# Optimization experiments

Hardware: AMD Instinct MI355X
Metric: run time of the kernel (lower is better)

## Reference

```python
import jax, jax.numpy as jnp
import numpy as np

B, S, D, H, W = 2, 2048, 1024, 16, 128
HD = D // H
EPS = 1e-5
NEG = -1e9


def setup_inputs() -> dict:
    key = jax.random.key(0)
    ks = jax.random.split(key, 6)
    sd = 1.0 / np.sqrt(D)
    return {
        "x": jax.random.normal(ks[0], (B, S, D), jnp.float32),
        "Wq": jax.random.normal(ks[1], (D, D), jnp.float32) * sd,
        "bq": jnp.zeros((D,), jnp.float32),
        "Wk": jax.random.normal(ks[2], (D, D), jnp.float32) * sd,
        "bk": jnp.zeros((D,), jnp.float32),
        "Wv": jax.random.normal(ks[3], (D, D), jnp.float32) * sd,
        "bv": jnp.zeros((D,), jnp.float32),
        "Wo": jax.random.normal(ks[4], (D, D), jnp.float32) * sd,
        "bo": jnp.zeros((D,), jnp.float32),
        "gamma": jnp.ones((D,), jnp.float32),
        "beta": jnp.zeros((D,), jnp.float32),
    }


def _local_causal_mask(seq_len, window):
    pos = jnp.arange(seq_len)
    qp = pos[:, None]
    kp = pos[None, :]
    return (jnp.abs(qp - kp) < window) & (qp >= kp)  # [S, S] bool


def reference(x, Wq, bq, Wk, bk, Wv, bv, Wo, bo, gamma, beta):
    scale = 1.0 / np.sqrt(HD)
    # projections -> [B, H, S, HD]
    def split_heads(t):
        return t.reshape(B, S, H, HD).transpose(0, 2, 1, 3)

    q = split_heads(x @ Wq + bq)
    k = split_heads(x @ Wk + bk)
    v = split_heads(x @ Wv + bv)

    scores = jnp.einsum("bhqd,bhkd->bhqk", q, k) * scale  # [B,H,S,S]
    mask = _local_causal_mask(S, W)
    scores = jnp.where(mask[None, None, :, :], scores, NEG)
    attn = jax.nn.softmax(scores, axis=-1)
    out = jnp.einsum("bhqk,bhkd->bhqd", attn, v)  # [B,H,S,HD]
    out = out.transpose(0, 2, 1, 3).reshape(B, S, D)
    out = out @ Wo + bo

    # residual + LayerNorm(eps=1e-5)
    y = x + out
    mu = jnp.mean(y, axis=-1, keepdims=True)
    var = jnp.mean(jnp.square(y - mu), axis=-1, keepdims=True)
    y = (y - mu) * jax.lax.rsqrt(var + EPS) * gamma + beta
    return y
```

## Files before the change

kernel.cpp:

```cpp
#include <hip/hip_runtime.h>
#include <hip/hip_bf16.h>

typedef __hip_bfloat16 bf16;
typedef float f32x4 __attribute__((ext_vector_type(4)));
typedef short bf16x8 __attribute__((ext_vector_type(8)));
typedef int   int4v  __attribute__((ext_vector_type(4)));

constexpr int Bb = 2, Ss = 2048, Dd = 1024, Hh = 16, Ww = 128, HDd = 64;
constexpr int Mrows = Bb * Ss;

__device__ __forceinline__ void gload16(const void* g, void* l) {
  __builtin_amdgcn_global_load_lds(
      (const __attribute__((address_space(1))) void*)g,
      (__attribute__((address_space(3))) void*)l, 16, 0, 0);
}

__device__ __forceinline__ f32x4 mfma16(bf16x8 a, bf16x8 b, f32x4 c) {
  return __builtin_amdgcn_mfma_f32_16x16x32_bf16(a, b, c, 0, 0, 0);
}

__global__ __launch_bounds__(256) void convert_bf16_k(const float* __restrict__ in,
                                                      bf16* __restrict__ out) {
  size_t i = (size_t)blockIdx.x * 256 + threadIdx.x;
  float4 v = reinterpret_cast<const float4*>(in)[i];
  union { bf16 b[4]; ushort4 u; } cv;
  cv.b[0] = __float2bfloat16(v.x);
  cv.b[1] = __float2bfloat16(v.y);
  cv.b[2] = __float2bfloat16(v.z);
  cv.b[3] = __float2bfloat16(v.w);
  reinterpret_cast<ushort4*>(out)[i] = cv.u;
}

__global__ __launch_bounds__(256) void transpose_w4_k(const float* __restrict__ W0,
                                                      const float* __restrict__ W1,
                                                      const float* __restrict__ W2,
                                                      const float* __restrict__ W3,
                                                      bf16* __restrict__ out) {
  const float* Win = (blockIdx.z == 0) ? W0 : (blockIdx.z == 1) ? W1
                     : (blockIdx.z == 2) ? W2 : W3;
  bf16* o = out + (size_t)blockIdx.z * Dd * Dd;
  __shared__ float tile[32][33];
  int bx = blockIdx.x, by = blockIdx.y;
  int tx = threadIdx.x & 31, ty = threadIdx.x >> 5;
#pragma unroll
  for (int i = 0; i < 4; ++i)
    tile[ty + i * 8][tx] = Win[(size_t)(by * 32 + ty + i * 8) * Dd + bx * 32 + tx];
  __syncthreads();
#pragma unroll
  for (int i = 0; i < 4; ++i)
    o[(size_t)(bx * 32 + ty + i * 8) * Dd + by * 32 + tx] =
        __float2bfloat16(tile[tx][ty + i * 8]);
}

__device__ __forceinline__ void gemm_core8(const bf16* __restrict__ A,
                                           const bf16* __restrict__ Bt,
                                           int bm, int bn,
                                           bf16* As, bf16* Bs, f32x4 acc[2][4]) {
  const int t = threadIdx.x;
  const int lane = t & 63, w = t >> 6;
  const int wr = w >> 1, wc = w & 1;
  const int l15 = lane & 15, l16 = lane >> 4;
  const bf16* Arow0 = A + (size_t)bm * 128 * Dd;
  const bf16* Brow0 = Bt + (size_t)bn * 128 * Dd;

  for (int kt = 0; kt < Dd / 64; ++kt) {
    __syncthreads();
#pragma unroll
    for (int i = 0; i < 2; ++i) {
      int ci = i * 512 + t;
      int row = ci >> 3, pc = ci & 7;
      int sc = pc ^ (row & 7);
      gload16(Arow0 + (size_t)row * Dd + kt * 64 + sc * 8, As + ci * 8);
      gload16(Brow0 + (size_t)row * Dd + kt * 64 + sc * 8, Bs + ci * 8);
    }
    __syncthreads();
    bf16x8 af[2][2], bfr[4][2];
#pragma unroll
    for (int m = 0; m < 2; ++m) {
      int row = wr * 32 + m * 16 + l15;
#pragma unroll
      for (int kk = 0; kk < 2; ++kk)
        af[m][kk] = *reinterpret_cast<const bf16x8*>(
            As + row * 64 + (((kk * 4 + l16) ^ (row & 7)) * 8));
    }
#pragma unroll
    for (int n = 0; n < 4; ++n) {
      int row = wc * 64 + n * 16 + l15;
#pragma unroll
      for (int kk = 0; kk < 2; ++kk)
        bfr[n][kk] = *reinterpret_cast<const bf16x8*>(
            Bs + row * 64 + (((kk * 4 + l16) ^ (row & 7)) * 8));
    }
    __builtin_amdgcn_s_setprio(1);
#pragma unroll
    for (int m = 0; m < 2; ++m)
#pragma unroll
      for (int n = 0; n < 4; ++n) {
        acc[m][n] = mfma16(af[m][0], bfr[n][0], acc[m][n]);
        acc[m][n] = mfma16(af[m][1], bfr[n][1], acc[m][n]);
      }
    __builtin_amdgcn_s_setprio(0);
  }
}

__global__ __launch_bounds__(512) void gemm_qkv8w(const bf16* __restrict__ A,
                                                  const bf16* __restrict__ Wt3,
                                                  const float* __restrict__ bq,
                                                  const float* __restrict__ bk,
                                                  const float* __restrict__ bv,
                                                  bf16* __restrict__ Qh,
                                                  bf16* __restrict__ Kh,
                                                  bf16* __restrict__ Vt) {
  __shared__ bf16 As[128 * 64], Bs[128 * 64];
  __shared__ bf16 rep[8][16][72];
  f32x4 acc[2][4] = {};
  int id = blockIdx.x;
  int wg = (id & 7) * 96 + (id >> 3);
  int bm = wg / 24, bn = wg % 24;
  gemm_core8(A, Wt3, bm, bn, As, Bs, acc);

  const int lane = threadIdx.x & 63, w = threadIdx.x >> 6;
  const int wr = w >> 1, wc = w & 1, l15 = lane & 15, l16 = lane >> 4;
  const int p = bn >> 3;
  const int c0w = (bn & 7) * 128 + wc * 64;
  const int h = c0w >> 6;

  if (p < 2) {
    bf16* dst = p ? Kh : Qh;
    const float* bp = p ? bk : bq;
    float bi[4];
#pragma unroll
    for (int n = 0; n < 4; ++n) bi[n] = bp[c0w + n * 16 + l15];
#pragma unroll
    for (int m = 0; m < 2; ++m) {
#pragma unroll
      for (int n = 0; n < 4; ++n)
#pragma unroll
        for (int r = 0; r < 4; ++r)
          rep[w][l16 * 4 + r][n * 16 + l15] = __float2bfloat16(acc[m][n][r] + bi[n]);
      int rrow = lane >> 2, rch = lane & 3;
      int sg = bm * 128 + wr * 32 + m * 16 + rrow;
      int b = sg >> 11, sl = sg & (Ss - 1);
      bf16* base = dst + (((size_t)(b * Hh + h)) * Ss + sl) * HDd;
      bf16x8 v0 = *reinterpret_cast<const bf16x8*>(&rep[w][rrow][rch * 8]);
      bf16x8 v1 = *reinterpret_cast<const bf16x8*>(&rep[w][rrow][(rch + 4) * 8]);
      *reinterpret_cast<bf16x8*>(base + rch * 8) = v0;
      *reinterpret_cast<bf16x8*>(base + (rch + 4) * 8) = v1;
    }
  } else {
#pragma unroll
    for (int n = 0; n < 4; ++n) {
      int col = c0w + n * 16 + l15;
      int hh = col >> 6, hd = col & (HDd - 1);
      float bi = bv[col];
#pragma unroll
      for (int m = 0; m < 2; ++m) {
        int s0 = bm * 128 + wr * 32 + m * 16 + l16 * 4;
        int b = s0 >> 11, sl = s0 & (Ss - 1);
        union { ushort4 u; ushort e[4]; } pk;
#pragma unroll
        for (int r = 0; r < 4; ++r) {
          bf16 tb = __float2bfloat16(acc[m][n][r] + bi);
          pk.e[r] = *reinterpret_cast<ushort*>(&tb);
        }
        *reinterpret_cast<ushort4*>(&Vt[(((size_t)(b * Hh + hh)) * HDd + hd) * Ss + sl]) = pk.u;
      }
    }
  }
}

__global__ __launch_bounds__(512) void gemm_o8w(const bf16* __restrict__ AO,
                                                const bf16* __restrict__ WtO,
                                                const float* __restrict__ bo,
                                                const float* __restrict__ resid,
                                                float* __restrict__ out) {
  __shared__ bf16 As[128 * 64], Bs[128 * 64];
  f32x4 acc[2][4] = {};
  int id = blockIdx.x;
  int wg = (id & 7) * 32 + (id >> 3);
  int bm = wg >> 3, bn = wg & 7;
  gemm_core8(AO, WtO, bm, bn, As, Bs, acc);

  const int lane = threadIdx.x & 63, w = threadIdx.x >> 6;
  const int wr = w >> 1, wc = w & 1, l15 = lane & 15, l16 = lane >> 4;
#pragma unroll
  for (int m = 0; m < 2; ++m)
#pragma unroll
    for (int n = 0; n < 4; ++n) {
      int col = bn * 128 + wc * 64 + n * 16 + l15;
      float bi = bo[col];
#pragma unroll
      for (int r = 0; r < 4; ++r) {
        int row = bm * 128 + wr * 32 + m * 16 + l16 * 4 + r;
        size_t idx = (size_t)row * Dd + col;
        out[idx] = acc[m][n][r] + bi + resid[idx];
      }
    }
}

__global__ __launch_bounds__(256) void attn_local(const bf16* __restrict__ Q,
                                                  const bf16* __restrict__ K,
                                                  const bf16* __restrict__ Vt,
                                                  bf16* __restrict__ AO) {
  __shared__ bf16 Ps[4][16][200];
  const int t = threadIdx.x, lane = t & 63, w = t >> 6;
  const int l15 = lane & 15, l16 = lane >> 4;
  const int qb = blockIdx.x, h = blockIdx.y, b = blockIdx.z;
  const int q0 = qb * 64, kstart = q0 - 128;
  const bf16* Qp = Q + ((size_t)(b * Hh + h)) * Ss * HDd;
  const bf16* Kp = K + ((size_t)(b * Hh + h)) * Ss * HDd;
  const bf16* Vp = Vt + ((size_t)(b * Hh + h)) * HDd * Ss;

  const int qrow = q0 + w * 16 + l15;
  bf16x8 aq0 = *reinterpret_cast<const bf16x8*>(Qp + (size_t)qrow * HDd + l16 * 8);
  bf16x8 aq1 = *reinterpret_cast<const bf16x8*>(Qp + (size_t)qrow * HDd + 32 + l16 * 8);

  f32x4 sc[9];
  __builtin_amdgcn_s_setprio(1);
#pragma unroll
  for (int j = 0; j < 9; ++j) {
    int key = kstart + (w + j) * 16 + l15;
    int kc = key < 0 ? 0 : key;
    bf16x8 bk0 = *reinterpret_cast<const bf16x8*>(Kp + (size_t)kc * HDd + l16 * 8);
    bf16x8 bk1 = *reinterpret_cast<const bf16x8*>(Kp + (size_t)kc * HDd + 32 + l16 * 8);
    f32x4 s = {};
    s = mfma16(aq0, bk0, s);
    s = mfma16(aq1, bk1, s);
    sc[j] = s;
  }
  __builtin_amdgcn_s_setprio(0);

  const float scale = 0.125f;
  float mrow[4], ssum[4], inv[4];
  int qg[4];
#pragma unroll
  for (int r = 0; r < 4; ++r) { mrow[r] = -1e30f; qg[r] = q0 + w * 16 + l16 * 4 + r; }
#pragma unroll
  for (int j = 0; j < 9; ++j) {
    int kg = kstart + (w + j) * 16 + l15;
#pragma unroll
    for (int r = 0; r < 4; ++r) {
      bool valid = (kg >= 0) && (kg <= qg[r]) && (qg[r] - kg < Ww);
      float v = valid ? sc[j][r] * scale : -1e9f;
      sc[j][r] = v;
      mrow[r] = fmaxf(mrow[r], v);
    }
  }
#pragma unroll
  for (int r = 0; r < 4; ++r)
#pragma unroll
    for (int off = 1; off < 16; off <<= 1)
      mrow[r] = fmaxf(mrow[r], __shfl_xor(mrow[r], off));
#pragma unroll
  for (int r = 0; r < 4; ++r) ssum[r] = 0.f;
#pragma unroll
  for (int j = 0; j < 9; ++j)
#pragma unroll
    for (int r = 0; r < 4; ++r) {
      float p = __expf(sc[j][r] - mrow[r]);
      sc[j][r] = p;
      ssum[r] += p;
    }
#pragma unroll
  for (int r = 0; r < 4; ++r)
#pragma unroll
    for (int off = 1; off < 16; off <<= 1)
      ssum[r] += __shfl_xor(ssum[r], off);
#pragma unroll
  for (int r = 0; r < 4; ++r) inv[r] = 1.f / ssum[r];

#pragma unroll
  for (int j = 0; j < 9; ++j)
#pragma unroll
    for (int r = 0; r < 4; ++r)
      Ps[w][l16 * 4 + r][(w + j) * 16 + l15] = __float2bfloat16(sc[j][r]);
  {
    int ktz = (w & 1) ? (w - 1) : (w + 9);
    bf16 z16 = __float2bfloat16(0.f);
#pragma unroll
    for (int r = 0; r < 4; ++r)
      Ps[w][l16 * 4 + r][ktz * 16 + l15] = z16;
  }

  const int c0 = w >> 1;
  f32x4 o[4] = {};
  __builtin_amdgcn_s_setprio(1);
#pragma unroll
  for (int cc = 0; cc < 5; ++cc) {
    int c = c0 + cc;
    bf16x8 pf = *reinterpret_cast<const bf16x8*>(&Ps[w][l15][c * 32 + l16 * 8]);
    int kk = kstart + c * 32 + l16 * 8;
    int kc = kk < 0 ? 0 : kk;
#pragma unroll
    for (int ht = 0; ht < 4; ++ht) {
      bf16x8 vf = *reinterpret_cast<const bf16x8*>(Vp + (size_t)(ht * 16 + l15) * Ss + kc);
      o[ht] = mfma16(pf, vf, o[ht]);
    }
  }
  __builtin_amdgcn_s_setprio(0);

#pragma unroll
  for (int ht = 0; ht < 4; ++ht)
#pragma unroll
    for (int r = 0; r < 4; ++r) {
      int qw = q0 + w * 16 + l16 * 4 + r;
      int col = h * HDd + ht * 16 + l15;
      AO[(size_t)(b * Ss + qw) * Dd + col] = __float2bfloat16(o[ht][r] * inv[r]);
    }
}

__global__ __launch_bounds__(256) void ln_inplace(float* __restrict__ y,
                                                  const float* __restrict__ gamma,
                                                  const float* __restrict__ beta) {
  int row = blockIdx.x;
  float* yr = y + (size_t)row * Dd;
  float4 v = reinterpret_cast<const float4*>(yr)[threadIdx.x];
  float s = v.x + v.y + v.z + v.w;
  float s2 = v.x * v.x + v.y * v.y + v.z * v.z + v.w * v.w;
#pragma unroll
  for (int off = 1; off < 64; off <<= 1) {
    s += __shfl_xor(s, off);
    s2 += __shfl_xor(s2, off);
  }
  __shared__ float r1[4], r2[4];
  int w = threadIdx.x >> 6;
  if ((threadIdx.x & 63) == 0) { r1[w] = s; r2[w] = s2; }
  __syncthreads();
  s = r1[0] + r1[1] + r1[2] + r1[3];
  s2 = r2[0] + r2[1] + r2[2] + r2[3];
  float mu = s * (1.f / Dd);
  float var = s2 * (1.f / Dd) - mu * mu;
  float rs = rsqrtf(var + 1e-5f);
  float4 g = reinterpret_cast<const float4*>(gamma)[threadIdx.x];
  float4 be = reinterpret_cast<const float4*>(beta)[threadIdx.x];
  float4 o;
  o.x = (v.x - mu) * rs * g.x + be.x;
  o.y = (v.y - mu) * rs * g.y + be.y;
  o.z = (v.z - mu) * rs * g.z + be.z;
  o.w = (v.w - mu) * rs * g.w + be.w;
  reinterpret_cast<float4*>(yr)[threadIdx.x] = o;
}

extern "C" void kernel_launch(void* const* d_in, const int* in_sizes, int n_in,
                              void* d_out, int out_size, void* d_ws, size_t ws_size,
                              hipStream_t stream) {
  const float* x     = (const float*)d_in[0];
  const float* Wq    = (const float*)d_in[1];
  const float* bq    = (const float*)d_in[2];
  const float* Wk    = (const float*)d_in[3];
  const float* bk    = (const float*)d_in[4];
  const float* Wv    = (const float*)d_in[5];
  const float* bv    = (const float*)d_in[6];
  const float* Wo    = (const float*)d_in[7];
  const float* bo    = (const float*)d_in[8];
  const float* gamma = (const float*)d_in[9];
  const float* beta  = (const float*)d_in[10];
  float* out = (float*)d_out;

  char* ws = (char*)d_ws;
  bf16* xb  = (bf16*)(ws + (size_t)0);
  bf16* Wt3 = (bf16*)(ws + ((size_t)8  << 20));
  bf16* WtO = (bf16*)(ws + ((size_t)14 << 20));
  bf16* Qh  = (bf16*)(ws + ((size_t)16 << 20));
  bf16* Kh  = (bf16*)(ws + ((size_t)24 << 20));
  bf16* Vt  = (bf16*)(ws + ((size_t)32 << 20));
  bf16* AO  = (bf16*)(ws + ((size_t)40 << 20));

  convert_bf16_k<<<Mrows * Dd / (256 * 4), 256, 0, stream>>>(x, xb);
  transpose_w4_k<<<dim3(32, 32, 4), 256, 0, stream>>>(Wq, Wk, Wv, Wo, Wt3);

  gemm_qkv8w<<<768, 512, 0, stream>>>(xb, Wt3, bq, bk, bv, Qh, Kh, Vt);

  attn_local<<<dim3(Ss / 64, Hh, Bb), 256, 0, stream>>>(Qh, Kh, Vt, AO);

  gemm_o8w<<<256, 512, 0, stream>>>(AO, WtO, bo, x, out);
  ln_inplace<<<Mrows, 256, 0, stream>>>(out, gamma, beta);
}
```

Before: 103.3 us.

## Double-buffer GEMM LDS tiles and prefetch V fragments before softmax

The shared GEMM core now uses two LDS buffers, issuing the global-to-LDS loads for the next K tile while MFMAs run on the current one, with one barrier per iteration instead of two. The QKV epilogue's staging buffer is carved out of the same LDS block. The attention kernel issues the first three chunks of V loads into registers before the softmax, so that load latency overlaps the masking and reduction work. In exchange LDS per block doubles to 64KB, which may lower occupancy, and the V prefetch adds 48 VGPRs.

Measured after the change: 98.83 us. 4.3% less time.

```diff
diff --git a/kernel.cpp b/kernel.cpp
--- a/kernel.cpp
+++ b/kernel.cpp
@@ -8,6 +8,7 @@
 
 constexpr int Bb = 2, Ss = 2048, Dd = 1024, Hh = 16, Ww = 128, HDd = 64;
 constexpr int Mrows = Bb * Ss;
+constexpr int NTk = Dd / 64;
 
 __device__ __forceinline__ void gload16(const void* g, void* l) {
   __builtin_amdgcn_global_load_lds(
@@ -55,7 +56,7 @@
 __device__ __forceinline__ void gemm_core8(const bf16* __restrict__ A,
                                            const bf16* __restrict__ Bt,
                                            int bm, int bn,
-                                           bf16* As, bf16* Bs, f32x4 acc[2][4]) {
+                                           bf16* lds, f32x4 acc[2][4]) {
   const int t = threadIdx.x;
   const int lane = t & 63, w = t >> 6;
   const int wr = w >> 1, wc = w & 1;
@@ -63,25 +64,32 @@
   const bf16* Arow0 = A + (size_t)bm * 128 * Dd;
   const bf16* Brow0 = Bt + (size_t)bn * 128 * Dd;
 
-  for (int kt = 0; kt < Dd / 64; ++kt) {
-    __syncthreads();
+  auto stage = [&](int buf, int kt) {
 #pragma unroll
     for (int i = 0; i < 2; ++i) {
       int ci = i * 512 + t;
       int row = ci >> 3, pc = ci & 7;
       int sc = pc ^ (row & 7);
-      gload16(Arow0 + (size_t)row * Dd + kt * 64 + sc * 8, As + ci * 8);
-      gload16(Brow0 + (size_t)row * Dd + kt * 64 + sc * 8, Bs + ci * 8);
-    }
-    __syncthreads();
+      gload16(Arow0 + (size_t)row * Dd + kt * 64 + sc * 8, lds + buf * 16384 + ci * 8);
+      gload16(Brow0 + (size_t)row * Dd + kt * 64 + sc * 8, lds + buf * 16384 + 8192 + ci * 8);
+    }
+  };
+
+  stage(0, 0);
+  __syncthreads();
+  int buf = 0;
+  for (int kt = 0; kt < NTk; ++kt) {
+    if (kt + 1 < NTk) stage(buf ^ 1, kt + 1);
     bf16x8 af[2][2], bfr[4][2];
+    const bf16* Ab = lds + buf * 16384;
+    const bf16* Bb = Ab + 8192;
 #pragma unroll
     for (int m = 0; m < 2; ++m) {
       int row = wr * 32 + m * 16 + l15;
 #pragma unroll
       for (int kk = 0; kk < 2; ++kk)
         af[m][kk] = *reinterpret_cast<const bf16x8*>(
-            As + row * 64 + (((kk * 4 + l16) ^ (row & 7)) * 8));
+            Ab + row * 64 + (((kk * 4 + l16) ^ (row & 7)) * 8));
     }
 #pragma unroll
     for (int n = 0; n < 4; ++n) {
@@ -89,7 +97,7 @@
 #pragma unroll
       for (int kk = 0; kk < 2; ++kk)
         bfr[n][kk] = *reinterpret_cast<const bf16x8*>(
-            Bs + row * 64 + (((kk * 4 + l16) ^ (row & 7)) * 8));
+            Bb + row * 64 + (((kk * 4 + l16) ^ (row & 7)) * 8));
     }
     __builtin_amdgcn_s_setprio(1);
 #pragma unroll
@@ -100,6 +108,8 @@
         acc[m][n] = mfma16(af[m][1], bfr[n][1], acc[m][n]);
       }
     __builtin_amdgcn_s_setprio(0);
+    __syncthreads();
+    buf ^= 1;
   }
 }
 
@@ -111,13 +121,12 @@
                                                   bf16* __restrict__ Qh,
                                                   bf16* __restrict__ Kh,
                                                   bf16* __restrict__ Vt) {
-  __shared__ bf16 As[128 * 64], Bs[128 * 64];
-  __shared__ bf16 rep[8][16][72];
+  __shared__ __align__(16) bf16 lds[32768];
   f32x4 acc[2][4] = {};
   int id = blockIdx.x;
   int wg = (id & 7) * 96 + (id >> 3);
   int bm = wg / 24, bn = wg % 24;
-  gemm_core8(A, Wt3, bm, bn, As, Bs, acc);
+  gemm_core8(A, Wt3, bm, bn, lds, acc);
 
   const int lane = threadIdx.x & 63, w = threadIdx.x >> 6;
   const int wr = w >> 1, wc = w & 1, l15 = lane & 15, l16 = lane >> 4;
@@ -126,6 +135,7 @@
   const int h = c0w >> 6;
 
   if (p < 2) {
+    bf16 (*rep)[72] = reinterpret_cast<bf16(*)[72]>(lds + w * (16 * 72));
     bf16* dst = p ? Kh : Qh;
     const float* bp = p ? bk : bq;
     float bi[4];
@@ -137,13 +147,13 @@
       for (int n = 0; n < 4; ++n)
 #pragma unroll
         for (int r = 0; r < 4; ++r)
-          rep[w][l16 * 4 + r][n * 16 + l15] = __float2bfloat16(acc[m][n][r] + bi[n]);
+          rep[l16 * 4 + r][n * 16 + l15] = __float2bfloat16(acc[m][n][r] + bi[n]);
       int rrow = lane >> 2, rch = lane & 3;
       int sg = bm * 128 + wr * 32 + m * 16 + rrow;
       int b = sg >> 11, sl = sg & (Ss - 1);
       bf16* base = dst + (((size_t)(b * Hh + h)) * Ss + sl) * HDd;
-      bf16x8 v0 = *reinterpret_cast<const bf16x8*>(&rep[w][rrow][rch * 8]);
-      bf16x8 v1 = *reinterpret_cast<const bf16x8*>(&rep[w][rrow][(rch + 4) * 8]);
+      bf16x8 v0 = *reinterpret_cast<const bf16x8*>(&rep[rrow][rch * 8]);
+      bf16x8 v1 = *reinterpret_cast<const bf16x8*>(&rep[rrow][(rch + 4) * 8]);
       *reinterpret_cast<bf16x8*>(base + rch * 8) = v0;
       *reinterpret_cast<bf16x8*>(base + (rch + 4) * 8) = v1;
     }
@@ -174,12 +184,12 @@
                                                 const float* __restrict__ bo,
                                                 const float* __restrict__ resid,
                                                 float* __restrict__ out) {
-  __shared__ bf16 As[128 * 64], Bs[128 * 64];
+  __shared__ __align__(16) bf16 lds[32768];
   f32x4 acc[2][4] = {};
   int id = blockIdx.x;
   int wg = (id & 7) * 32 + (id >> 3);
   int bm = wg >> 3, bn = wg & 7;
-  gemm_core8(AO, WtO, bm, bn, As, Bs, acc);
+  gemm_core8(AO, WtO, bm, bn, lds, acc);
 
   const int lane = threadIdx.x & 63, w = threadIdx.x >> 6;
   const int wr = w >> 1, wc = w & 1, l15 = lane & 15, l16 = lane >> 4;
@@ -230,6 +240,17 @@
   }
   __builtin_amdgcn_s_setprio(0);
 
+  const int c0 = w >> 1;
+  bf16x8 vpre[3][4];
+#pragma unroll
+  for (int cc = 0; cc < 3; ++cc) {
+    int kk = kstart + (c0 + cc) * 32 + l16 * 8;
+    int kc = kk < 0 ? 0 : kk;
+#pragma unroll
+    for (int ht = 0; ht < 4; ++ht)
+      vpre[cc][ht] = *reinterpret_cast<const bf16x8*>(Vp + (size_t)(ht * 16 + l15) * Ss + kc);
+  }
+
   const float scale = 0.125f;
   float mrow[4], ssum[4], inv[4];
   int qg[4];
@@ -282,19 +303,24 @@
       Ps[w][l16 * 4 + r][ktz * 16 + l15] = z16;
   }
 
-  const int c0 = w >> 1;
   f32x4 o[4] = {};
   __builtin_amdgcn_s_setprio(1);
 #pragma unroll
   for (int cc = 0; cc < 5; ++cc) {
     int c = c0 + cc;
     bf16x8 pf = *reinterpret_cast<const bf16x8*>(&Ps[w][l15][c * 32 + l16 * 8]);
-    int kk = kstart + c * 32 + l16 * 8;
-    int kc = kk < 0 ? 0 : kk;
-#pragma unroll
-    for (int ht = 0; ht < 4; ++ht) {
-      bf16x8 vf = *reinterpret_cast<const bf16x8*>(Vp + (size_t)(ht * 16 + l15) * Ss + kc);
-      o[ht] = mfma16(pf, vf, o[ht]);
+    if (cc < 3) {
+#pragma unroll
+      for (int ht = 0; ht < 4; ++ht)
+        o[ht] = mfma16(pf, vpre[cc][ht], o[ht]);
+    } else {
+      int kk = kstart + c * 32 + l16 * 8;
+      int kc = kk < 0 ? 0 : kk;
+#pragma unroll
+      for (int ht = 0; ht < 4; ++ht) {
+        bf16x8 vf = *reinterpret_cast<const bf16x8*>(Vp + (size_t)(ht * 16 + l15) * Ss + kc);
+        o[ht] = mfma16(pf, vf, o[ht]);
+      }
     }
   }
   __builtin_amdgcn_s_setprio(0);
```
